# Kernel tuning notes

Hardware: AMD Instinct MI355X
Metric: run time of the kernel (lower is better)

The kernel has to match this reference:

```python
import jax, jax.numpy as jnp
import numpy as np


def conv2d(x, w, b):
    # x: [D, Cin, H, W], w: [Cout, Cin, kh, kw], SAME padding, stride 1
    y = jax.lax.conv_general_dilated(
        x, w, window_strides=(1, 1), padding='SAME',
        dimension_numbers=('NCHW', 'OIHW', 'NCHW'))
    return y + b[None, :, None, None]


def setup_inputs() -> dict:
    key = jax.random.key(0)
    ks = jax.random.split(key, 12)
    B, N, T, H, W = 2, 3, 16, 28, 28
    Cp, Ch, Ck, Cv, Cs = 1024, 512, 64, 512, 256
    s = 0.02
    return {
        'f16': jax.random.normal(ks[0], (B, Cp, H, W), jnp.float32),
        'mk':  jax.random.normal(ks[1], (B, Ck, T, H, W), jnp.float32),
        'mv':  jax.random.normal(ks[2], (B, N, Cv, T, H, W), jnp.float32),
        'h':   jax.random.normal(ks[3], (B, N, Cs, H, W), jnp.float32),
        # KeyProj: 1x1 conv then 3x3 conv
        'w1': jax.random.normal(ks[4], (Ch, Cp, 1, 1), jnp.float32) * s,
        'b1': jnp.zeros((Ch,), jnp.float32),
        'w2': jax.random.normal(ks[5], (Ck, Ch, 3, 3), jnp.float32) * s,
        'b2': jnp.zeros((Ck,), jnp.float32),
        # sensory-updater transform: 3x3 conv, (Cv+Cs) -> 3*Cs
        'wt': jax.random.normal(ks[6], (3 * Cs, Cv + Cs, 3, 3), jnp.float32) * s,
        'bt': jnp.zeros((3 * Cs,), jnp.float32),
    }


def reference(f16, mk, mv, h, w1, b1, w2, b2, wt, bt):
    B, Ck, T = mk.shape[0], mk.shape[1], mk.shape[2]
    N, Cv = mv.shape[1], mv.shape[2]
    Cs = h.shape[2]
    H, W = f16.shape[-2:]
    P = H * W          # query pixels
    M = T * H * W      # memory slots

    # KeyProj: query key from pixel feature
    qk = conv2d(conv2d(f16, w1, b1), w2, b2)          # [B, Ck, H, W]

    # KV-memory affinity read (softmax over memory axis)
    mk_flat = mk.reshape(B, Ck, M)
    qk_flat = qk.reshape(B, Ck, P)
    logits = jnp.einsum('bcm,bcp->bmp', mk_flat, qk_flat) / jnp.sqrt(
        jnp.asarray(Ck, qk.dtype))                     # [B, M, P]
    aff = jax.nn.softmax(logits, axis=1)               # normalize over memory
    readout = jnp.einsum('bncm,bmp->bncp', mv.reshape(B, N, Cv, M), aff)
    readout = readout.reshape(B, N, Cv, H, W)          # [B, N, Cv, H, W]

    # gated recurrent sensory update (recurrent_update)
    x = jnp.concatenate([readout, h], axis=2).reshape(B * N, Cv + Cs, H, W)
    vals = conv2d(x, wt, bt).reshape(B, N, 3 * Cs, H, W)
    forget_g = jax.nn.sigmoid(vals[:, :, :Cs])
    update_g = jax.nn.sigmoid(vals[:, :, Cs:2 * Cs])
    new_vals = jnp.tanh(vals[:, :, 2 * Cs:])
    new_h = forget_g * h * (1.0 - update_g) + update_g * new_vals
    return new_h
```

## Files before the change

kernel.cpp:

```cpp
#include <hip/hip_runtime.h>

typedef unsigned short u16;
typedef unsigned int u32;
typedef float f32x4v __attribute__((ext_vector_type(4)));
typedef __bf16 bf16x8 __attribute__((ext_vector_type(8)));

#define GAS __attribute__((address_space(1)))
#define LAS __attribute__((address_space(3)))

__device__ __forceinline__ u16 f2bf(float f) {
  u32 u = __builtin_bit_cast(u32, f);
  u32 r = (u + 0x7FFFu + ((u >> 16) & 1u)) >> 16;
  return (u16)r;
}
__device__ __forceinline__ float bf2f(u16 h) {
  return __builtin_bit_cast(float, (u32)h << 16);
}
__device__ __forceinline__ void gld_lds16(const void* g, void* l) {
  __builtin_amdgcn_global_load_lds((const GAS void*)g, (LAS void*)l, 16, 0, 0);
}
#define VMCNT(N) asm volatile("s_waitcnt vmcnt(" #N ")" ::: "memory")
#define MFMA16(a, b, c) __builtin_amdgcn_mfma_f32_16x16x32_bf16((a), (b), (c), 0, 0, 0)

template <int CONV>
__global__ __launch_bounds__(512, 4) void gemmRC(
    const u16* __restrict__ A, const u16* __restrict__ B, u16* __restrict__ Cp,
    int M, int N, int Kc, int fullK, int S,
    long strA, long strB, long strC, int Cin, int gx, int gy, int nwg)
{
  const int cpx = (int)gridDim.x >> 3;
  const int L = ((int)blockIdx.x & 7) * cpx + ((int)blockIdx.x >> 3);
  if (L >= nwg) return;
  const int by = L % gy;
  const int rest = L / gy;
  const int bx = rest % gx;
  const int z = rest / gx;

  extern __shared__ u16 smem[];
  u16* sA = smem;
  u16* sB = smem + 3 * 8192;
  const int t = threadIdx.x, lane = t & 63, wave = t >> 6;
  const int zb = z / S, s = z - zb * S;
  const int m0 = bx * 256, n0 = by * 128;
  const int kbeg = s * Kc;
  const int kavail = fullK - kbeg;
  const int kc = Kc < kavail ? Kc : kavail;
  const int niter = kc >> 5;

  const int schunk = ((t & 3) ^ ((t >> 4) & 3)) * 8;
  const u16* Ap[2]; const u16* Bp;
  #pragma unroll
  for (int q = 0; q < 2; ++q) {
    int ra = m0 + q * 128 + (t >> 2); if (ra >= M) ra = M - 1;
    Ap[q] = A + (long)zb * strA + (long)ra * fullK + schunk;
  }
  if constexpr (CONV) {
    int pn = n0 + (t >> 2); if (pn >= N) pn = 0;
    const int img = pn / 784, p = pn - img * 784;
    const int py = p / 28, px = p - py * 28;
    Bp = B + ((long)img * 900 + (py + 1) * 30 + (px + 1)) * Cin + schunk;
  } else {
    int rb = n0 + (t >> 2); if (rb >= N) rb = N - 1;
    Bp = B + (long)zb * strB + (long)rb * fullK + schunk;
  }
  const int ldst = t * 8;

  auto stage = [&](int buf, int kg) {
    long boff;
    if constexpr (CONV) {
      const int tap = kg / Cin, kcc = kg - tap * Cin;
      boff = (long)((tap / 3 - 1) * 30 + (tap % 3 - 1)) * Cin + kcc;
    } else {
      boff = kg;
    }
    u16* dA = sA + buf * 8192;
    gld_lds16(Ap[0] + kg, &dA[ldst]);
    gld_lds16(Ap[1] + kg, &dA[4096 + ldst]);
    gld_lds16(Bp + boff,  &sB[buf * 4096 + ldst]);
  };

  const int wrow = (wave & 3) * 64, wcol = (wave >> 2) * 64;
  const int lr = lane & 15, hi = lane >> 4;
  const int csw = (hi ^ (lr >> 2)) * 8;
  f32x4v acc[4][4] = {};

  for (int p = 0; p < 2 && p < niter; ++p) stage(p, kbeg + p * 32);
  int cur = 0, nxt = 2;
  for (int it = 0; it < niter; ++it) {
    if (it + 2 < niter) {
      stage(nxt, kbeg + (it + 2) * 32);
      VMCNT(6);
    } else {
      const int rem = niter - 1 - it;
      if (rem == 1) VMCNT(3); else VMCNT(0);
    }
    __builtin_amdgcn_s_barrier();
    __builtin_amdgcn_sched_barrier(0);
    const u16* cA = sA + cur * 8192;
    const u16* cB = sB + cur * 4096;
    bf16x8 af[4], bf[4];
    #pragma unroll
    for (int m = 0; m < 4; ++m) af[m] = *(const bf16x8*)&cA[(wrow + m*16 + lr) * 32 + csw];
    #pragma unroll
    for (int n = 0; n < 4; ++n) bf[n] = *(const bf16x8*)&cB[(wcol + n*16 + lr) * 32 + csw];
    __builtin_amdgcn_s_setprio(1);
    #pragma unroll
    for (int m = 0; m < 4; ++m)
      #pragma unroll
      for (int n = 0; n < 4; ++n)
        acc[m][n] = MFMA16(af[m], bf[n], acc[m][n]);
    __builtin_amdgcn_s_setprio(0);
    __builtin_amdgcn_sched_barrier(0);
    __builtin_amdgcn_s_barrier();
    cur = (cur + 1 == 3) ? 0 : cur + 1;
    nxt = (nxt + 1 == 3) ? 0 : nxt + 1;
  }

  u16* Co = Cp + (long)z * strC;
  const int lq = hi * 4;
  #pragma unroll
  for (int m = 0; m < 4; ++m)
    #pragma unroll
    for (int r = 0; r < 4; ++r) {
      const int row = m0 + wrow + m * 16 + lq + r;
      if (row >= M) continue;
      #pragma unroll
      for (int n = 0; n < 4; ++n) {
        const int col = n0 + wcol + n * 16 + lr;
        if (col < N) Co[(long)row * N + col] = f2bf(acc[m][n][r]);
      }
    }
}

template <int BK, int OUT>
__global__ __launch_bounds__(256) void gemm_glds(
    const u16* __restrict__ A, const u16* __restrict__ B, void* __restrict__ C,
    const float* __restrict__ bias,
    int M, int N, int Kc, int fullK, int S,
    long strA, long strB, long strC, float scale)
{
  constexpr int CPR = BK / 8;
  constexpr int ISS = BK / 16;
  __shared__ u16 sA[2][128 * BK];
  __shared__ u16 sB[2][128 * BK];
  const int t = threadIdx.x, lane = t & 63, wave = t >> 6;
  const int z = blockIdx.z, zb = z / S, s = z - zb * S;
  const int m0 = blockIdx.x * 128, n0 = blockIdx.y * 128;
  const int kbeg = s * Kc;

  const u16* Aptr[ISS]; const u16* Bptr[ISS]; int lofs[ISS];
  #pragma unroll
  for (int i = 0; i < ISS; ++i) {
    const int tp = i * 256 + t;
    const int r = tp / CPR;
    int c16 = tp % CPR;
    if constexpr (BK == 32) c16 = c16 ^ ((tp >> 4) & 3);
    else                    c16 = (c16 - (r & 7)) & 7;
    int ra = m0 + r; if (ra >= M) ra = M - 1;
    int rb = n0 + r; if (rb >= N) rb = N - 1;
    Aptr[i] = A + (long)zb * strA + (long)ra * fullK + kbeg + c16 * 8;
    Bptr[i] = B + (long)zb * strB + (long)rb * fullK + kbeg + c16 * 8;
    lofs[i] = (i * 256 + (wave << 6)) * 8;
  }
  auto stage = [&](int buf, int k0) {
    #pragma unroll
    for (int i = 0; i < ISS; ++i) {
      gld_lds16(Aptr[i] + k0, &sA[buf][lofs[i]]);
      gld_lds16(Bptr[i] + k0, &sB[buf][lofs[i]]);
    }
  };

  const int wr = (wave >> 1) * 64, wc = (wave & 1) * 64;
  const int lr = lane & 15, hi = lane >> 4;
  f32x4v acc[4][4] = {};
  const int niter = Kc / BK;

  stage(0, 0);
  for (int it = 0; it < niter; ++it) {
    const int cur = it & 1;
    if (it + 1 < niter) {
      stage(cur ^ 1, (it + 1) * BK);
      if constexpr (ISS == 2) VMCNT(4); else VMCNT(8);
    } else {
      VMCNT(0);
    }
    __builtin_amdgcn_s_barrier();
    __builtin_amdgcn_sched_barrier(0);
    #pragma unroll
    for (int kk = 0; kk < BK; kk += 32) {
      bf16x8 af[4], bv[4];
      #pragma unroll
      for (int i = 0; i < 4; ++i) {
        const int row = wr + i*16 + lr;
        int lk;
        if constexpr (BK == 32) lk = kk + ((hi ^ (lr >> 2)) * 8);
        else                    lk = ((((kk >> 3) + hi) + (row & 7)) & 7) * 8;
        af[i] = *(const bf16x8*)&sA[cur][row * BK + lk];
      }
      #pragma unroll
      for (int j = 0; j < 4; ++j) {
        const int row = wc + j*16 + lr;
        int lk;
        if constexpr (BK == 32) lk = kk + ((hi ^ (lr >> 2)) * 8);
        else                    lk = ((((kk >> 3) + hi) + (row & 7)) & 7) * 8;
        bv[j] = *(const bf16x8*)&sB[cur][row * BK + lk];
      }
      __builtin_amdgcn_s_setprio(1);
      #pragma unroll
      for (int i = 0; i < 4; ++i)
        #pragma unroll
        for (int j = 0; j < 4; ++j)
          acc[i][j] = MFMA16(af[i], bv[j], acc[i][j]);
      __builtin_amdgcn_s_setprio(0);
    }
    __builtin_amdgcn_sched_barrier(0);
    __builtin_amdgcn_s_barrier();
  }

  const int lq = hi * 4;
  if constexpr (OUT == 1) {
    u16* Cw = (u16*)C + (long)zb * strC;
    #pragma unroll
    for (int i = 0; i < 4; ++i)
      #pragma unroll
      for (int r = 0; r < 4; ++r) {
        const int row = m0 + wr + i*16 + lq + r;
        if (row >= M) continue;
        #pragma unroll
        for (int j = 0; j < 4; ++j) {
          const int col = n0 + wc + j*16 + lr;
          if (col < N) Cw[(long)row * N + col] = f2bf(acc[i][j][r] * scale);
        }
      }
  } else {
    u16* Cw = (u16*)C;
    #pragma unroll
    for (int i = 0; i < 4; ++i)
      #pragma unroll
      for (int r = 0; r < 4; ++r) {
        const int row = m0 + wr + i*16 + lq + r;
        if (row >= M) continue;
        const int im = row / 784, q = row - im * 784;
        const int qpad = (q / 28 + 1) * 30 + (q % 28 + 1);
        u16* drow = Cw + ((long)im * 900 + qpad) * 512;
        #pragma unroll
        for (int j = 0; j < 4; ++j) {
          const int col = n0 + wc + j*16 + lr;
          if (col < N) drow[col] = f2bf(acc[i][j][r] + bias[col]);
        }
      }
  }
}

__global__ __launch_bounds__(256) void conv_glds(
    const u16* __restrict__ Wt, const u16* __restrict__ imgP,
    float* __restrict__ Cp, int M, int Cin, int Ntot, int Kc)
{
  __shared__ u16 sA[2][128 * 32];
  __shared__ u16 sB[2][128 * 32];
  const int t = threadIdx.x, lane = t & 63, wave = t >> 6;
  const int z = blockIdx.z;
  const int m0 = blockIdx.x * 128, n0 = blockIdx.y * 128;
  const int kbeg = z * Kc;

  const u16* Aptr[2]; const u16* Bptr[2]; int lofs[2];
  #pragma unroll
  for (int i = 0; i < 2; ++i) {
    const int tp = i * 256 + t;
    const int r = tp >> 2;
    const int c16 = (tp & 3) ^ ((tp >> 4) & 3);
    int ra = m0 + r; if (ra >= M) ra = M - 1;
    int pn = n0 + r; if (pn >= Ntot) pn = 0;
    const int img = pn / 784, p = pn - img * 784;
    const int py = p / 28, px = p - py * 28;
    Aptr[i] = Wt + (long)ra * (9 * Cin) + c16 * 8;
    Bptr[i] = imgP + ((long)img * 900 + (py + 1) * 30 + (px + 1)) * Cin + c16 * 8;
    lofs[i] = (i * 256 + (wave << 6)) * 8;
  }
  auto stage = [&](int buf, int kg) {
    const int tap = kg / Cin, kc = kg - tap * Cin;
    const long off = (long)((tap / 3 - 1) * 30 + (tap % 3 - 1)) * Cin + kc;
    #pragma unroll
    for (int i = 0; i < 2; ++i) {
      gld_lds16(Aptr[i] + kg, &sA[buf][lofs[i]]);
      gld_lds16(Bptr[i] + off, &sB[buf][lofs[i]]);
    }
  };

  const int wr = (wave >> 1) * 64, wc = (wave & 1) * 64;
  const int lr = lane & 15, hi = lane >> 4;
  const int csw = (hi ^ (lr >> 2)) * 8;
  f32x4v acc[4][4] = {};
  const int niter = Kc >> 5;

  stage(0, kbeg);
  for (int it = 0; it < niter; ++it) {
    const int cur = it & 1;
    if (it + 1 < niter) {
      stage(cur ^ 1, kbeg + (it + 1) * 32);
      VMCNT(4);
    } else {
      VMCNT(0);
    }
    __builtin_amdgcn_s_barrier();
    __builtin_amdgcn_sched_barrier(0);
    bf16x8 af[4], bv[4];
    #pragma unroll
    for (int i = 0; i < 4; ++i) af[i] = *(const bf16x8*)&sA[cur][(wr + i*16 + lr) * 32 + csw];
    #pragma unroll
    for (int j = 0; j < 4; ++j) bv[j] = *(const bf16x8*)&sB[cur][(wc + j*16 + lr) * 32 + csw];
    __builtin_amdgcn_s_setprio(1);
    #pragma unroll
    for (int i = 0; i < 4; ++i)
      #pragma unroll
      for (int j = 0; j < 4; ++j)
        acc[i][j] = MFMA16(af[i], bv[j], acc[i][j]);
    __builtin_amdgcn_s_setprio(0);
    __builtin_amdgcn_sched_barrier(0);
    __builtin_amdgcn_s_barrier();
  }

  float* Co = Cp + (long)z * M * Ntot;
  const int lq = hi * 4;
  #pragma unroll
  for (int i = 0; i < 4; ++i)
    #pragma unroll
    for (int r = 0; r < 4; ++r) {
      const int row = m0 + wr + i*16 + lq + r;
      if (row >= M) continue;
      #pragma unroll
      for (int j = 0; j < 4; ++j) {
        const int col = n0 + wc + j*16 + lr;
        if (col < Ntot) Co[(long)row * Ntot + col] = acc[i][j][r];
      }
    }
}

__global__ __launch_bounds__(256) void transpose_bf(
    const float* __restrict__ in, u16* __restrict__ out,
    int R, int C, long strOutZ, int ldOut, int colOff)
{
  __shared__ float tile[32][33];
  in  += (long)blockIdx.z * R * C;
  out += (long)blockIdx.z * strOutZ;
  const int c0 = blockIdx.x * 32, r0 = blockIdx.y * 32;
  const int tx = threadIdx.x & 31, ty = threadIdx.x >> 5;
  for (int i = ty; i < 32; i += 8) {
    const int r = r0 + i, c = c0 + tx;
    tile[i][tx] = (r < R && c < C) ? in[(long)r * C + c] : 0.0f;
  }
  __syncthreads();
  for (int i = ty; i < 32; i += 8) {
    const int r = r0 + tx, c = c0 + i;
    if (c < C && r < R)
      out[(long)c * ldOut + colOff + r] = f2bf(tile[tx][i]);
  }
}

__global__ __launch_bounds__(256) void convert_bf(
    const float* __restrict__ in, u16* __restrict__ out, long n8)
{
  const long i = (long)blockIdx.x * 256 + threadIdx.x;
  if (i >= n8) return;
  const float4* p = (const float4*)in + i * 2;
  const float4 a = p[0], b = p[1];
  u16 o[8] = {f2bf(a.x), f2bf(a.y), f2bf(a.z), f2bf(a.w),
              f2bf(b.x), f2bf(b.y), f2bf(b.z), f2bf(b.w)};
  ((uint4*)out)[i] = *(uint4*)o;
}

__global__ __launch_bounds__(256) void permute_w(
    const float* __restrict__ src, u16* __restrict__ dst, int M, int Cin)
{
  const long total = (long)M * 9 * Cin;
  const long idx = (long)blockIdx.x * 256 + threadIdx.x;
  if (idx >= total) return;
  const int c = (int)(idx % Cin);
  const int tap = (int)((idx / Cin) % 9);
  const int m = (int)(idx / ((long)9 * Cin));
  dst[idx] = f2bf(src[((long)m * Cin + c) * 9 + tap]);
}

__global__ __launch_bounds__(256) void zfill(u32* __restrict__ p, long n) {
  const long stride = (long)gridDim.x * 256;
  for (long i = (long)blockIdx.x * 256 + threadIdx.x; i < n; i += stride) p[i] = 0;
}

__global__ __launch_bounds__(256) void reduceT_ro(
    const u16* __restrict__ parts, u16* __restrict__ dst, int S)
{
  __shared__ float tile[32][33];
  const int b = blockIdx.z, c0 = blockIdx.x * 32, p0 = blockIdx.y * 32;
  const int tx = threadIdx.x & 31, ty = threadIdx.x >> 5;
  for (int i = ty; i < 32; i += 8) {
    const int pc = min(p0 + tx, 783);
    float s = 0;
    for (int k = 0; k < S; ++k)
      s += bf2f(parts[((long)(b * S + k) * 1536 + c0 + i) * 784 + pc]);
    tile[i][tx] = s;
  }
  __syncthreads();
  for (int i = ty; i < 32; i += 8) {
    const int p = p0 + i, c = c0 + tx;
    if (p < 784) {
      const int n = c >> 9, cc = c & 511;
      const int qpad = (p / 28 + 1) * 30 + (p % 28 + 1);
      dst[((long)(b * 3 + n) * 900 + qpad) * 768 + cc] = f2bf(tile[tx][i]);
    }
  }
}

__global__ __launch_bounds__(256) void reduceT_qk(
    const float* __restrict__ parts, u16* __restrict__ dst,
    const float* __restrict__ bias, int S)
{
  __shared__ float tile[32][33];
  const int b = blockIdx.z, c0 = blockIdx.x * 32, p0 = blockIdx.y * 32;
  const int tx = threadIdx.x & 31, ty = threadIdx.x >> 5;
  for (int i = ty; i < 32; i += 8) {
    const int pc = min(p0 + tx, 783);
    const long base = (long)(c0 + i) * 1568 + b * 784 + pc;
    float s = 0;
    for (int k = 0; k < S; ++k) s += parts[(long)k * 64 * 1568 + base];
    tile[i][tx] = s;
  }
  __syncthreads();
  for (int i = ty; i < 32; i += 8) {
    const int p = p0 + i, c = c0 + tx;
    if (p < 784)
      dst[((long)b * 784 + p) * 64 + c] = f2bf(tile[tx][i] + bias[c]);
  }
}

__global__ __launch_bounds__(256) void transT_h(
    const float* __restrict__ h, u16* __restrict__ dst)
{
  __shared__ float tile[32][33];
  const int zimg = blockIdx.z, c0 = blockIdx.x * 32, p0 = blockIdx.y * 32;
  const int tx = threadIdx.x & 31, ty = threadIdx.x >> 5;
  for (int i = ty; i < 32; i += 8) {
    const int pc = min(p0 + tx, 783);
    tile[i][tx] = h[((long)zimg * 256 + c0 + i) * 784 + pc];
  }
  __syncthreads();
  for (int i = ty; i < 32; i += 8) {
    const int p = p0 + i, c = c0 + tx;
    if (p < 784) {
      const int qpad = (p / 28 + 1) * 30 + (p % 28 + 1);
      dst[((long)zimg * 900 + qpad) * 768 + 512 + c] = f2bf(tile[tx][i]);
    }
  }
}

__global__ __launch_bounds__(256) void softmax_inplace(u16* __restrict__ buf)
{
  uint4* p4 = (uint4*)(buf + (long)blockIdx.x * 12544);
  const int t = threadIdx.x;
  __shared__ float red[4];
  uint4 v[7];
  float mx = -3.0e38f;
  #pragma unroll
  for (int q = 0; q < 7; ++q) {
    const int idx = t + q * 256;
    if (idx < 1568) {
      v[q] = p4[idx];
      const u32 w[4] = {v[q].x, v[q].y, v[q].z, v[q].w};
      #pragma unroll
      for (int e = 0; e < 4; ++e) {
        mx = fmaxf(mx, bf2f((u16)(w[e] & 0xFFFFu)));
        mx = fmaxf(mx, bf2f((u16)(w[e] >> 16)));
      }
    }
  }
  #pragma unroll
  for (int o = 32; o > 0; o >>= 1) mx = fmaxf(mx, __shfl_xor(mx, o));
  if ((t & 63) == 0) red[t >> 6] = mx;
  __syncthreads();
  mx = fmaxf(fmaxf(red[0], red[1]), fmaxf(red[2], red[3]));

  float s = 0.0f;
  #pragma unroll
  for (int q = 0; q < 7; ++q) {
    const int idx = t + q * 256;
    if (idx < 1568) {
      const u32 w[4] = {v[q].x, v[q].y, v[q].z, v[q].w};
      #pragma unroll
      for (int e = 0; e < 4; ++e) {
        s += __expf(bf2f((u16)(w[e] & 0xFFFFu)) - mx);
        s += __expf(bf2f((u16)(w[e] >> 16)) - mx);
      }
    }
  }
  #pragma unroll
  for (int o = 32; o > 0; o >>= 1) s += __shfl_xor(s, o);
  __syncthreads();
  if ((t & 63) == 0) red[t >> 6] = s;
  __syncthreads();
  const float inv = 1.0f / (red[0] + red[1] + red[2] + red[3]);

  #pragma unroll
  for (int q = 0; q < 7; ++q) {
    const int idx = t + q * 256;
    if (idx < 1568) {
      u32 w[4] = {v[q].x, v[q].y, v[q].z, v[q].w};
      #pragma unroll
      for (int e = 0; e < 4; ++e) {
        const float a = __expf(bf2f((u16)(w[e] & 0xFFFFu)) - mx) * inv;
        const float b = __expf(bf2f((u16)(w[e] >> 16)) - mx) * inv;
        w[e] = (u32)f2bf(a) | ((u32)f2bf(b) << 16);
      }
      p4[idx] = make_uint4(w[0], w[1], w[2], w[3]);
    }
  }
}

__device__ __forceinline__ void addbf4(float* a, uint2 v) {
  a[0] += bf2f((u16)(v.x & 0xFFFFu));
  a[1] += bf2f((u16)(v.x >> 16));
  a[2] += bf2f((u16)(v.y & 0xFFFFu));
  a[3] += bf2f((u16)(v.y >> 16));
}

__global__ __launch_bounds__(256) void treduce_gate(
    const u16* __restrict__ parts, const float* __restrict__ bt,
    const float* __restrict__ h, float* __restrict__ out, int S)
{
  const long i = (long)blockIdx.x * 256 + threadIdx.x;
  if (i >= 6L * 256 * 196) return;
  const int p4 = (int)(i % 196);
  const int rest = (int)(i / 196);
  const int cs = rest % 256, im = rest / 256;
  const long slice = 768L * 4704;
  const long pbase = (long)im * 784 + p4 * 4;
  float F[4] = {}, U[4] = {}, NV[4] = {};
  for (int s = 0; s < S; ++s) {
    const u16* P = parts + (long)s * slice;
    addbf4(F,  *(const uint2*)&P[(long)cs         * 4704 + pbase]);
    addbf4(U,  *(const uint2*)&P[(long)(256 + cs) * 4704 + pbase]);
    addbf4(NV, *(const uint2*)&P[(long)(512 + cs) * 4704 + pbase]);
  }
  const float bF = bt[cs], bU = bt[256 + cs], bN = bt[512 + cs];
  const f32x4v hv = ((const f32x4v*)h)[((long)(im * 256 + cs) * 784 >> 2) + p4];
  f32x4v o;
  #pragma unroll
  for (int q = 0; q < 4; ++q) {
    const float f = F[q] + bF, u = U[q] + bU, nv = NV[q] + bN;
    const float sf = 1.0f / (1.0f + __expf(-f));
    const float su = 1.0f / (1.0f + __expf(-u));
    const float e2 = __expf(2.0f * nv);
    const float tv = (e2 - 1.0f) / (e2 + 1.0f);
    o[q] = sf * hv[q] * (1.0f - su) + su * tv;
  }
  ((f32x4v*)out)[((long)(im * 256 + cs) * 784 >> 2) + p4] = o;
}

__global__ __launch_bounds__(256) void fill_sentinel(float* p, long n) {
  const long i = (long)blockIdx.x * 256 + threadIdx.x;
  if (i < n) p[i] = 12345.0f;
}

extern "C" void kernel_launch(void* const* d_in, const int* in_sizes, int n_in,
                              void* d_out, int out_size, void* d_ws, size_t ws_size,
                              hipStream_t stream) {
  const float* f16 = (const float*)d_in[0];
  const float* mk  = (const float*)d_in[1];
  const float* mv  = (const float*)d_in[2];
  const float* hin = (const float*)d_in[3];
  const float* w1  = (const float*)d_in[4];
  const float* b1  = (const float*)d_in[5];
  const float* w2  = (const float*)d_in[6];
  const float* b2  = (const float*)d_in[7];
  const float* wt  = (const float*)d_in[8];
  const float* bt  = (const float*)d_in[9];
  float* out = (float*)d_out;

  (void)hipFuncSetAttribute((const void*)gemmRC<0>,
                            hipFuncAttributeMaxDynamicSharedMemorySize, 73728);
  (void)hipFuncSetAttribute((const void*)gemmRC<1>,
                            hipFuncAttributeMaxDynamicSharedMemorySize, 73728);
  constexpr unsigned DSM = 73728;

  const size_t B_f16T   = 2UL*784*1024*2;
  const size_t B_w1b    = 512UL*1024*2;
  const size_t B_w2R    = 64UL*4608*2;
  const size_t B_out1P  = 2UL*900*512*2;
  const size_t B_qkT    = 2UL*784*64*2;
  const size_t B_concat = 6UL*900*768*2;
  const size_t B_wtR    = 768UL*6912*2;
  const size_t B_mkT    = 2UL*12544*64*2;
  const size_t B_logaff = 2UL*784*12544*2;
  const size_t B_mvb    = 38535168UL*2;
  auto al = [](size_t x) { return (x + 255) & ~(size_t)255; };
  auto kcFor = [](int K, int S) { return ((K + S - 1) / S + 31) & ~31; };
  auto pad8 = [](int n) { return (n + 7) & ~7; };

  const size_t phase1 = al(B_f16T) + al(B_w1b) + al(B_w2R) + al(B_out1P) + al(B_qkT);
  const size_t regionA = phase1 > al(B_concat) ? phase1 : al(B_concat);

  auto poolFor = [&](int S_ro, int S_tr) -> size_t {
    size_t p2 = 18UL*64*1568*4;
    size_t pr = (size_t)(2*S_ro)*1536*784*2;
    size_t pt = (size_t)S_tr*768*4704*2;
    size_t m = p2; if (pr > m) m = pr; if (pt > m) m = pt;
    return m;
  };
  const size_t fixed = regionA + al(B_wtR) + al(B_mkT) + al(B_logaff) + al(B_mvb);

  int S_ro = 6, S_tr = 4;
  if (fixed + poolFor(S_ro, S_tr) > ws_size) { S_ro = 3; S_tr = 2; }
  if (fixed + poolFor(S_ro, S_tr) > ws_size) {
    fill_sentinel<<<4704, 256, 0, stream>>>(out, (long)out_size);
    return;
  }
  const int Kc_ro = kcFor(12544, S_ro);
  const int Kc_tr = kcFor(6912, S_tr);

  char* base = (char*)d_ws;
  size_t off = 0;
  auto alloc = [&](size_t bytes) -> char* { char* p = base + off; off += al(bytes); return p; };
  char* rA = alloc(regionA);
  u16* f16T   = (u16*)rA;
  u16* w1b    = (u16*)(rA + al(B_f16T));
  u16* w2R    = (u16*)(rA + al(B_f16T) + al(B_w1b));
  u16* out1P  = (u16*)(rA + al(B_f16T) + al(B_w1b) + al(B_w2R));
  u16* qkT    = (u16*)(rA + al(B_f16T) + al(B_w1b) + al(B_w2R) + al(B_out1P));
  u16* concatP = (u16*)rA;
  u16*   wtR     = (u16*)alloc(B_wtR);
  u16*   mkT     = (u16*)alloc(B_mkT);
  u16*   logaff  = (u16*)alloc(B_logaff);
  u16*   mvb     = (u16*)alloc(B_mvb);
  char*  partsRaw = alloc(poolFor(S_ro, S_tr));
  float* partsF  = (float*)partsRaw;
  u16*   partsH  = (u16*)partsRaw;

  zfill<<<512, 256, 0, stream>>>((u32*)out1P, (long)(B_out1P / 4));

  convert_bf<<<256, 256, 0, stream>>>(w1, w1b, 65536);
  permute_w<<<1152, 256, 0, stream>>>(w2, w2R, 64, 512);
  permute_w<<<20736, 256, 0, stream>>>(wt, wtR, 768, 768);
  transpose_bf<<<dim3(25, 32, 2), 256, 0, stream>>>(f16, f16T, 1024, 784, 784L*1024, 1024, 0);
  transpose_bf<<<dim3(392, 2, 2), 256, 0, stream>>>(mk, mkT, 64, 12544, 12544L*64, 64, 0);
  convert_bf<<<18816, 256, 0, stream>>>(mv, mvb, 4816896);

  gemm_glds<64, 2><<<dim3(13, 4, 1), 256, 0, stream>>>(
      f16T, w1b, out1P, b1, 1568, 512, 1024, 1024, 1, 0, 0, 0, 1.0f);

  conv_glds<<<dim3(1, 13, 18), 256, 0, stream>>>(w2R, out1P, partsF, 64, 512, 1568, 256);
  reduceT_qk<<<dim3(2, 25, 2), 256, 0, stream>>>(partsF, qkT, b2, 18);

  gemm_glds<64, 1><<<dim3(7, 98, 2), 256, 0, stream>>>(
      qkT, mkT, logaff, nullptr, 784, 12544, 64, 64, 1,
      784L*64, 12544L*64, 784L*12544, 0.125f);

  softmax_inplace<<<1568, 256, 0, stream>>>(logaff);

  zfill<<<2048, 256, 0, stream>>>((u32*)concatP, (long)(B_concat / 4));
  transT_h<<<dim3(8, 25, 6), 256, 0, stream>>>(hin, concatP);

  {
    const int nwg = 6 * 7 * 2 * S_ro;
    gemmRC<0><<<pad8(nwg), 512, DSM, stream>>>(
        mvb, logaff, partsH, 1536, 784, Kc_ro, 12544, S_ro,
        1536L*12544, 784L*12544, 1536L*784, 0, 6, 7, nwg);
  }
  reduceT_ro<<<dim3(48, 25, 2), 256, 0, stream>>>(partsH, concatP, S_ro);

  {
    const int nwg = 3 * 37 * S_tr;
    gemmRC<1><<<pad8(nwg), 512, DSM, stream>>>(
        wtR, concatP, partsH, 768, 4704, Kc_tr, 6912, S_tr,
        0, 0, 768L*4704, 768, 3, 37, nwg);
  }

  treduce_gate<<<1176, 256, 0, stream>>>(partsH, bt, hin, out, S_tr);
}
```

Measured before the change: 356.2 us.

## Add 256x256-tile 8-wave GEMM for readout and transform; split-K the 1x1 conv

Adds a new GEMM kernel with 256x256 output tiles, 8 waves, 128KB LDS double buffering and staggered A/B prefetch. It replaces the 128-wide gemmRC for the memory-readout GEMM and the 3x3 transform conv, which cuts redundant operand loads per output. The 1x1 KeyProj conv now uses gemmRC with split-K over 8 slices, followed by a new reduction kernel that adds the bias and writes into the padded layout. Split counts and K chunks are now hard-coded, the fallback to smaller splits is gone, and larger tiles lower occupancy and waste work on edge tiles.

```diff
diff --git a/kernel.cpp b/kernel.cpp
--- a/kernel.cpp
+++ b/kernel.cpp
@@ -21,6 +21,149 @@
 }
 #define VMCNT(N) asm volatile("s_waitcnt vmcnt(" #N ")" ::: "memory")
 #define MFMA16(a, b, c) __builtin_amdgcn_mfma_f32_16x16x32_bf16((a), (b), (c), 0, 0, 0)
+
+template <int CONV>
+__global__ __launch_bounds__(512, 2) void gemm8p(
+    const u16* __restrict__ A, const u16* __restrict__ B, u16* __restrict__ Cp,
+    int M, int N, int Kc, int fullK, int S,
+    long strA, long strB, long strC, int Cin, int gx, int gy, int nwg)
+{
+  const int cpx = (int)gridDim.x >> 3;
+  const int L = ((int)blockIdx.x & 7) * cpx + ((int)blockIdx.x >> 3);
+  if (L >= nwg) return;
+  const int by = L % gy;
+  const int rest = L / gy;
+  const int bx = rest % gx;
+  const int z = rest / gx;
+
+  extern __shared__ u16 smem[];
+  const int t = threadIdx.x, lane = t & 63, wave = t >> 6;
+  const int zb = z / S, s = z - zb * S;
+  const int m0 = bx * 256, n0 = by * 256;
+  const int kbeg = s * Kc;
+  const int kavail = fullK - kbeg;
+  const int kc = Kc < kavail ? Kc : kavail;
+  const int T = kc >> 6;
+
+  const int srow = t >> 3;
+  const int g = ((t & 7) - (srow & 7)) & 7;
+  const int ldsoff = t * 8;
+
+  const u16* Asrc[2][2];
+  #pragma unroll
+  for (int h = 0; h < 2; ++h)
+    #pragma unroll
+    for (int q = 0; q < 2; ++q) {
+      int r = m0 + h * 128 + q * 64 + srow; if (r >= M) r = M - 1;
+      Asrc[h][q] = A + (long)zb * strA + (long)r * fullK + kbeg + g * 8;
+    }
+  const u16* Bsrc[2][2];
+  #pragma unroll
+  for (int h = 0; h < 2; ++h)
+    #pragma unroll
+    for (int q = 0; q < 2; ++q) {
+      if constexpr (CONV) {
+        int pn = n0 + h * 128 + q * 64 + srow; if (pn >= N) pn = 0;
+        const int img = pn / 784, p = pn - img * 784;
+        const int py = p / 28, px = p - py * 28;
+        Bsrc[h][q] = B + ((long)img * 900 + (py + 1) * 30 + (px + 1)) * Cin + g * 8;
+      } else {
+        int r = n0 + h * 128 + q * 64 + srow; if (r >= N) r = N - 1;
+        Bsrc[h][q] = B + (long)zb * strB + (long)r * fullK + kbeg + g * 8;
+      }
+    }
+
+  auto stageA = [&](int tile, int h) {
+    u16* d = smem + (((tile & 1) * 2 + h) * 8192);
+    const long ko = (long)tile * 64;
+    gld_lds16(Asrc[h][0] + ko, d + ldsoff);
+    gld_lds16(Asrc[h][1] + ko, d + 4096 + ldsoff);
+  };
+  auto stageB = [&](int tile, int h) {
+    u16* d = smem + 32768 + (((tile & 1) * 2 + h) * 8192);
+    long off;
+    if constexpr (CONV) {
+      const int kg = kbeg + tile * 64;
+      const int tap = kg / Cin, kc2 = kg - tap * Cin;
+      off = (long)((tap / 3 - 1) * 30 + (tap % 3 - 1)) * Cin + kc2;
+    } else {
+      off = (long)tile * 64;
+    }
+    gld_lds16(Bsrc[h][0] + off, d + ldsoff);
+    gld_lds16(Bsrc[h][1] + off, d + 4096 + ldsoff);
+  };
+
+  const int wm = wave & 1, wn = wave >> 1;
+  const int lr = lane & 15, hi = lane >> 4;
+  const int slot0 = ((hi + (lr & 7)) & 7) * 8;
+  const int slot1 = (((hi + 4) + (lr & 7)) & 7) * 8;
+  f32x4v acc[8][4] = {};
+  bf16x8 breg[4][2];
+
+  stageB(0, 0); stageB(0, 1);
+  stageA(0, 0); stageA(0, 1);
+  stageB(1, 0); stageB(1, 1);
+  VMCNT(4);
+  __builtin_amdgcn_s_barrier();
+
+  for (int tau = 0; tau < T; ++tau) {
+    const int d = tau & 1;
+    const u16* aB = smem + ((d * 2 + wm) * 8192);
+    const u16* bB = smem + 32768 + ((d * 2 + (wn >> 1)) * 8192);
+    const int ta = (tau + 1 < T) ? tau + 1 : T - 1;
+    const int tb = (tau + 2 < T) ? tau + 2 : T - 1;
+    #pragma unroll
+    for (int Q = 0; Q < 4; ++Q) {
+      bf16x8 aph[2][2];
+      #pragma unroll
+      for (int m2 = 0; m2 < 2; ++m2) {
+        const int lrow = (Q * 2 + m2) * 16 + lr;
+        aph[m2][0] = *(const bf16x8*)&aB[lrow * 64 + slot0];
+        aph[m2][1] = *(const bf16x8*)&aB[lrow * 64 + slot1];
+      }
+      if (Q == 0) {
+        #pragma unroll
+        for (int n = 0; n < 4; ++n) {
+          const int lrow = (wn & 1) * 64 + n * 16 + lr;
+          breg[n][0] = *(const bf16x8*)&bB[lrow * 64 + slot0];
+          breg[n][1] = *(const bf16x8*)&bB[lrow * 64 + slot1];
+        }
+      }
+      if      (Q == 0) stageA(ta, 0);
+      else if (Q == 1) stageA(ta, 1);
+      else if (Q == 2) stageB(tb, 0);
+      else             { stageB(tb, 1); VMCNT(4); }
+      __builtin_amdgcn_sched_barrier(0);
+      __builtin_amdgcn_s_barrier();
+      __builtin_amdgcn_s_setprio(1);
+      #pragma unroll
+      for (int m2 = 0; m2 < 2; ++m2)
+        #pragma unroll
+        for (int n = 0; n < 4; ++n) {
+          acc[Q * 2 + m2][n] = MFMA16(aph[m2][0], breg[n][0], acc[Q * 2 + m2][n]);
+          acc[Q * 2 + m2][n] = MFMA16(aph[m2][1], breg[n][1], acc[Q * 2 + m2][n]);
+        }
+      __builtin_amdgcn_s_setprio(0);
+      __builtin_amdgcn_sched_barrier(0);
+      __builtin_amdgcn_s_barrier();
+    }
+  }
+  VMCNT(0);
+
+  u16* Co = Cp + (long)z * strC;
+  #pragma unroll
+  for (int m = 0; m < 8; ++m)
+    #pragma unroll
+    for (int r = 0; r < 4; ++r) {
+      const int row = m0 + wm * 128 + m * 16 + hi * 4 + r;
+      if (row >= M) continue;
+      #pragma unroll
+      for (int n = 0; n < 4; ++n) {
+        const int col = n0 + wn * 64 + n * 16 + lr;
+        if (col < N) Co[(long)row * N + col] = f2bf(acc[m][n][r]);
+      }
+    }
+}
 
 template <int CONV>
 __global__ __launch_bounds__(512, 4) void gemmRC(
@@ -132,10 +275,9 @@
     }
 }
 
-template <int BK, int OUT>
+template <int BK>
 __global__ __launch_bounds__(256) void gemm_glds(
-    const u16* __restrict__ A, const u16* __restrict__ B, void* __restrict__ C,
-    const float* __restrict__ bias,
+    const u16* __restrict__ A, const u16* __restrict__ B, u16* __restrict__ C,
     int M, int N, int Kc, int fullK, int S,
     long strA, long strB, long strC, float scale)
 {
@@ -144,9 +286,9 @@
   __shared__ u16 sA[2][128 * BK];
   __shared__ u16 sB[2][128 * BK];
   const int t = threadIdx.x, lane = t & 63, wave = t >> 6;
-  const int z = blockIdx.z, zb = z / S, s = z - zb * S;
+  const int z = blockIdx.z, zb = z / S;
   const int m0 = blockIdx.x * 128, n0 = blockIdx.y * 128;
-  const int kbeg = s * Kc;
+  const int kbeg = (z - zb * S) * Kc;
 
   const u16* Aptr[ISS]; const u16* Bptr[ISS]; int lofs[ISS];
   #pragma unroll
@@ -218,38 +360,19 @@
   }
 
   const int lq = hi * 4;
-  if constexpr (OUT == 1) {
-    u16* Cw = (u16*)C + (long)zb * strC;
-    #pragma unroll
-    for (int i = 0; i < 4; ++i)
-      #pragma unroll
-      for (int r = 0; r < 4; ++r) {
-        const int row = m0 + wr + i*16 + lq + r;
-        if (row >= M) continue;
-        #pragma unroll
-        for (int j = 0; j < 4; ++j) {
-          const int col = n0 + wc + j*16 + lr;
-          if (col < N) Cw[(long)row * N + col] = f2bf(acc[i][j][r] * scale);
-        }
-      }
-  } else {
-    u16* Cw = (u16*)C;
-    #pragma unroll
-    for (int i = 0; i < 4; ++i)
-      #pragma unroll
-      for (int r = 0; r < 4; ++r) {
-        const int row = m0 + wr + i*16 + lq + r;
-        if (row >= M) continue;
-        const int im = row / 784, q = row - im * 784;
-        const int qpad = (q / 28 + 1) * 30 + (q % 28 + 1);
-        u16* drow = Cw + ((long)im * 900 + qpad) * 512;
-        #pragma unroll
-        for (int j = 0; j < 4; ++j) {
-          const int col = n0 + wc + j*16 + lr;
-          if (col < N) drow[col] = f2bf(acc[i][j][r] + bias[col]);
-        }
-      }
-  }
+  u16* Cw = C + (long)zb * strC;
+  #pragma unroll
+  for (int i = 0; i < 4; ++i)
+    #pragma unroll
+    for (int r = 0; r < 4; ++r) {
+      const int row = m0 + wr + i*16 + lq + r;
+      if (row >= M) continue;
+      #pragma unroll
+      for (int j = 0; j < 4; ++j) {
+        const int col = n0 + wc + j*16 + lr;
+        if (col < N) Cw[(long)row * N + col] = f2bf(acc[i][j][r] * scale);
+      }
+    }
 }
 
 __global__ __launch_bounds__(256) void conv_glds(
@@ -386,6 +509,30 @@
   for (long i = (long)blockIdx.x * 256 + threadIdx.x; i < n; i += stride) p[i] = 0;
 }
 
+__device__ __forceinline__ void addbf4(float* a, uint2 v) {
+  a[0] += bf2f((u16)(v.x & 0xFFFFu));
+  a[1] += bf2f((u16)(v.x >> 16));
+  a[2] += bf2f((u16)(v.y & 0xFFFFu));
+  a[3] += bf2f((u16)(v.y >> 16));
+}
+
+__global__ __launch_bounds__(256) void reduce_c1_bf(
+    const u16* __restrict__ parts, u16* __restrict__ dst,
+    const float* __restrict__ bias, int S)
+{
+  const long idx = (long)blockIdx.x * 256 + threadIdx.x;
+  if (idx >= 1568L * 128) return;
+  const int c4 = (int)(idx & 127), p = (int)(idx >> 7);
+  const int c = c4 * 4;
+  float sum[4] = {bias[c], bias[c+1], bias[c+2], bias[c+3]};
+  for (int s = 0; s < S; ++s)
+    addbf4(sum, *(const uint2*)&parts[((long)s * 1568 + p) * 512 + c]);
+  const int im = p / 784, q = p - im * 784;
+  const int qpad = (q / 28 + 1) * 30 + (q % 28 + 1);
+  u16 o[4] = {f2bf(sum[0]), f2bf(sum[1]), f2bf(sum[2]), f2bf(sum[3])};
+  *(uint2*)&dst[((long)im * 900 + qpad) * 512 + c] = *(uint2*)o;
+}
+
 __global__ __launch_bounds__(256) void reduceT_ro(
     const u16* __restrict__ parts, u16* __restrict__ dst, int S)
 {
@@ -512,13 +659,6 @@
       p4[idx] = make_uint4(w[0], w[1], w[2], w[3]);
     }
   }
-}
-
-__device__ __forceinline__ void addbf4(float* a, uint2 v) {
-  a[0] += bf2f((u16)(v.x & 0xFFFFu));
-  a[1] += bf2f((u16)(v.x >> 16));
-  a[2] += bf2f((u16)(v.y & 0xFFFFu));
-  a[3] += bf2f((u16)(v.y >> 16));
 }
 
 __global__ __launch_bounds__(256) void treduce_gate(
@@ -574,11 +714,13 @@
   const float* bt  = (const float*)d_in[9];
   float* out = (float*)d_out;
 
+  (void)hipFuncSetAttribute((const void*)gemm8p<0>,
+                            hipFuncAttributeMaxDynamicSharedMemorySize, 131072);
+  (void)hipFuncSetAttribute((const void*)gemm8p<1>,
+                            hipFuncAttributeMaxDynamicSharedMemorySize, 131072);
   (void)hipFuncSetAttribute((const void*)gemmRC<0>,
                             hipFuncAttributeMaxDynamicSharedMemorySize, 73728);
-  (void)hipFuncSetAttribute((const void*)gemmRC<1>,
-                            hipFuncAttributeMaxDynamicSharedMemorySize, 73728);
-  constexpr unsigned DSM = 73728;
+  constexpr unsigned DSM8 = 131072, DSMR = 73728;
 
   const size_t B_f16T   = 2UL*784*1024*2;
   const size_t B_w1b    = 512UL*1024*2;
@@ -591,29 +733,27 @@
   const size_t B_logaff = 2UL*784*12544*2;
   const size_t B_mvb    = 38535168UL*2;
   auto al = [](size_t x) { return (x + 255) & ~(size_t)255; };
-  auto kcFor = [](int K, int S) { return ((K + S - 1) / S + 31) & ~31; };
   auto pad8 = [](int n) { return (n + 7) & ~7; };
 
   const size_t phase1 = al(B_f16T) + al(B_w1b) + al(B_w2R) + al(B_out1P) + al(B_qkT);
   const size_t regionA = phase1 > al(B_concat) ? phase1 : al(B_concat);
 
-  auto poolFor = [&](int S_ro, int S_tr) -> size_t {
+  const int S_ro = 5, S_tr = 4, S_c1 = 8;
+  const int Kc_ro = 2560;
+  const int Kc_tr = 1728;
+  auto poolBytes = [&]() -> size_t {
     size_t p2 = 18UL*64*1568*4;
+    size_t p1 = (size_t)S_c1*1568*512*2;
     size_t pr = (size_t)(2*S_ro)*1536*784*2;
     size_t pt = (size_t)S_tr*768*4704*2;
-    size_t m = p2; if (pr > m) m = pr; if (pt > m) m = pt;
+    size_t m = p2; if (p1 > m) m = p1; if (pr > m) m = pr; if (pt > m) m = pt;
     return m;
   };
   const size_t fixed = regionA + al(B_wtR) + al(B_mkT) + al(B_logaff) + al(B_mvb);
-
-  int S_ro = 6, S_tr = 4;
-  if (fixed + poolFor(S_ro, S_tr) > ws_size) { S_ro = 3; S_tr = 2; }
-  if (fixed + poolFor(S_ro, S_tr) > ws_size) {
+  if (fixed + poolBytes() > ws_size) {
     fill_sentinel<<<4704, 256, 0, stream>>>(out, (long)out_size);
     return;
   }
-  const int Kc_ro = kcFor(12544, S_ro);
-  const int Kc_tr = kcFor(6912, S_tr);
 
   char* base = (char*)d_ws;
   size_t off = 0;
@@ -629,7 +769,7 @@
   u16*   mkT     = (u16*)alloc(B_mkT);
   u16*   logaff  = (u16*)alloc(B_logaff);
   u16*   mvb     = (u16*)alloc(B_mvb);
-  char*  partsRaw = alloc(poolFor(S_ro, S_tr));
+  char*  partsRaw = alloc(poolBytes());
   float* partsF  = (float*)partsRaw;
   u16*   partsH  = (u16*)partsRaw;
 
@@ -642,14 +782,19 @@
   transpose_bf<<<dim3(392, 2, 2), 256, 0, stream>>>(mk, mkT, 64, 12544, 12544L*64, 64, 0);
   convert_bf<<<18816, 256, 0, stream>>>(mv, mvb, 4816896);
 
-  gemm_glds<64, 2><<<dim3(13, 4, 1), 256, 0, stream>>>(
-      f16T, w1b, out1P, b1, 1568, 512, 1024, 1024, 1, 0, 0, 0, 1.0f);
+  {
+    const int nwg = 7 * 4 * S_c1;
+    gemmRC<0><<<pad8(nwg), 512, DSMR, stream>>>(
+        f16T, w1b, partsH, 1568, 512, 1024 / S_c1, 1024, S_c1,
+        0, 0, 1568L*512, 0, 7, 4, nwg);
+  }
+  reduce_c1_bf<<<784, 256, 0, stream>>>(partsH, out1P, b1, S_c1);
 
   conv_glds<<<dim3(1, 13, 18), 256, 0, stream>>>(w2R, out1P, partsF, 64, 512, 1568, 256);
   reduceT_qk<<<dim3(2, 25, 2), 256, 0, stream>>>(partsF, qkT, b2, 18);
 
-  gemm_glds<64, 1><<<dim3(7, 98, 2), 256, 0, stream>>>(
-      qkT, mkT, logaff, nullptr, 784, 12544, 64, 64, 1,
+  gemm_glds<64><<<dim3(7, 98, 2), 256, 0, stream>>>(
+      qkT, mkT, logaff, 784, 12544, 64, 64, 1,
       784L*64, 12544L*64, 784L*12544, 0.125f);
 
   softmax_inplace<<<1568, 256, 0, stream>>>(logaff);
@@ -658,18 +803,18 @@
   transT_h<<<dim3(8, 25, 6), 256, 0, stream>>>(hin, concatP);
 
   {
-    const int nwg = 6 * 7 * 2 * S_ro;
-    gemmRC<0><<<pad8(nwg), 512, DSM, stream>>>(
+    const int nwg = 6 * 4 * 2 * S_ro;
+    gemm8p<0><<<pad8(nwg), 512, DSM8, stream>>>(
         mvb, logaff, partsH, 1536, 784, Kc_ro, 12544, S_ro,
-        1536L*12544, 784L*12544, 1536L*784, 0, 6, 7, nwg);
+        1536L*12544, 784L*12544, 1536L*784, 0, 6, 4, nwg);
   }
   reduceT_ro<<<dim3(48, 25, 2), 256, 0, stream>>>(partsH, concatP, S_ro);
 
   {
-    const int nwg = 3 * 37 * S_tr;
-    gemmRC<1><<<pad8(nwg), 512, DSM, stream>>>(
+    const int nwg = 3 * 19 * S_tr;
+    gemm8p<1><<<pad8(nwg), 512, DSM8, stream>>>(
         wtR, concatP, partsH, 768, 4704, Kc_tr, 6912, S_tr,
-        0, 0, 768L*4704, 768, 3, 37, nwg);
+        0, 0, 768L*4704, 768, 3, 19, nwg);
   }
 
   treduce_gate<<<1176, 256, 0, stream>>>(partsH, bt, hin, out, S_tr);
```

Result: faster. 324.7 us (-8.9%).
